# Optimization experiments

Measured on AMD Instinct MI355X. Metric: run time of the kernel, lower is better.

## Reference

```python
import jax, jax.numpy as jnp
import numpy as np

D_MODEL = 1024
NUM_HEADS = 16
HEAD_DIM = D_MODEL // NUM_HEADS


def setup_inputs() -> dict:
    key = jax.random.key(0)
    ks = jax.random.split(key, 5)
    s = 1.0 / np.sqrt(D_MODEL)
    return {
        "x": jax.random.normal(ks[0], (2, 2048, D_MODEL), dtype=jnp.float32),
        "Wqkv": jax.random.normal(ks[1], (3 * D_MODEL, D_MODEL), dtype=jnp.float32) * s,
        "bqkv": jax.random.normal(ks[2], (3 * D_MODEL,), dtype=jnp.float32) * s,
        "Wo": jax.random.normal(ks[3], (D_MODEL, D_MODEL), dtype=jnp.float32) * s,
        "bo": jax.random.normal(ks[4], (D_MODEL,), dtype=jnp.float32) * s,
    }


def reference(x, Wqkv, bqkv, Wo, bo):
    B, S, D = x.shape
    H, hd = NUM_HEADS, HEAD_DIM
    # fused QKV projection (torch Linear: x @ W.T + b)
    qkv = x @ Wqkv.T + bqkv                      # [B, S, 3D]
    qkv = qkv.reshape(B, S, H, 3 * hd).transpose(0, 2, 1, 3)  # [B, H, S, 3hd]
    q, k, v = jnp.split(qkv, 3, axis=-1)         # each [B, H, S, hd]
    scaled = jnp.einsum("bhqd,bhkd->bhqk", q, k) / jnp.sqrt(jnp.float32(hd))
    # module applies causal mask when its `mask` flag is False (the default)
    causal = jnp.tril(jnp.ones((S, S), dtype=bool))
    scaled = jnp.where(causal, scaled, -jnp.inf)
    attn = jax.nn.softmax(scaled, axis=-1)       # [B, H, S, S]
    values = jnp.einsum("bhqk,bhkd->bhqd", attn, v)  # [B, H, S, hd]
    # NOTE: original uses .reshape (not transpose-then-reshape) on the
    # [B, H, S, hd] tensor directly — reproduce that exact layout.
    values = values.reshape(B, S, H * hd)
    out = values @ Wo.T + bo                     # [B, S, D]
    return out
```

## Files before the change

### kernel.cpp

```cpp
#include <hip/hip_runtime.h>

typedef __attribute__((ext_vector_type(8))) short bf16x8;
typedef __attribute__((ext_vector_type(4))) float f32x4;

#define D_MODEL 1024
#define NHEADS 16
#define HDIM 64
#define SEQ 2048
#define BATCH 2
#define MROWS (BATCH*SEQ)
#define NQKV (3*D_MODEL)
#define QSCALE 0.1803368801111204f
#define CSTR 144

__device__ __forceinline__ unsigned short f2bf(float f) {
  unsigned int u = __float_as_uint(f);
  u += 0x7FFF + ((u >> 16) & 1);
  return (unsigned short)(u >> 16);
}
__device__ __forceinline__ unsigned int pack2bf(float a, float b) {
#if __has_builtin(__builtin_amdgcn_cvt_pk_bf16_f32)
  auto r = __builtin_amdgcn_cvt_pk_bf16_f32(a, b);
  unsigned int u; __builtin_memcpy(&u, &r, 4);
  return u;
#else
  return ((unsigned int)f2bf(b) << 16) | (unsigned int)f2bf(a);
#endif
}

__device__ __forceinline__ void gload16(const void* g, void* l) {
  __builtin_amdgcn_global_load_lds((const __attribute__((address_space(1))) void*)g,
                                   (__attribute__((address_space(3))) void*)l, 16, 0, 0);
}

#define N4_X     1048576
#define N4_WQKV   786432
#define N4_WO     262144
__global__ void cvt_all_kernel(const float4* __restrict__ x,
                               const float4* __restrict__ wqkv,
                               const float4* __restrict__ wo,
                               ushort4* __restrict__ xb,
                               ushort4* __restrict__ wqkvb,
                               ushort4* __restrict__ wob) {
  int i = blockIdx.x * blockDim.x + threadIdx.x;
  const float4* s; ushort4* d; int j;
  if (i < N4_X)                { s = x;    d = xb;    j = i; }
  else if (i < N4_X + N4_WQKV) { s = wqkv; d = wqkvb; j = i - N4_X; }
  else                         { s = wo;   d = wob;   j = i - (N4_X + N4_WQKV); }
  float4 v = s[j];
  ushort4 o;
  o.x = f2bf(v.x); o.y = f2bf(v.y); o.z = f2bf(v.z); o.w = f2bf(v.w);
  d[j] = o;
}

template<int MODE, int BM>
__global__ __launch_bounds__(256) void gemm_bt_kernel(
    const unsigned short* __restrict__ A,
    const unsigned short* __restrict__ Bm,
    const float* __restrict__ bias,
    float* __restrict__ outF,
    unsigned short* __restrict__ Qb,
    unsigned short* __restrict__ Kb,
    unsigned short* __restrict__ VTb,
    int M, int N, int K)
{
  constexpr int MI = BM / 32;
  constexpr int STG = BM*32 + 128*32;
  constexpr int SHSZ = (MODE == 0 && 128*CSTR > 2*STG) ? 128*CSTR : 2*STG;
  __shared__ __align__(16) unsigned short Sh[SHSZ];
  const int tid = threadIdx.x;
  const int wave = tid >> 6, lane = tid & 63;
  const int lm = lane & 15, quad = lane >> 4;
  const int wm = (wave >> 1) * (BM/2), wn = (wave & 1) * 64;
  const int m0 = blockIdx.y * BM, n0 = blockIdx.x * 128;

  f32x4 acc[MI][4] = {};

  auto stage_in = [&](int k0, int sb) {
    unsigned short* As = Sh + sb*STG;
    unsigned short* Bs = As + BM*32;
#pragma unroll
    for (int i = 0; i < BM/64; i++) {
      int ch = i*256 + tid;
      int r = ch >> 2, cg = (ch & 3) ^ ((r >> 1) & 3);
      gload16(&A[(size_t)(m0 + r) * K + k0 + cg*8], &As[ch*8]);
    }
#pragma unroll
    for (int i = 0; i < 2; i++) {
      int ch = i*256 + tid;
      int r = ch >> 2, cg = (ch & 3) ^ ((r >> 1) & 3);
      gload16(&Bm[(size_t)(n0 + r) * K + k0 + cg*8], &Bs[ch*8]);
    }
  };

  stage_in(0, 0);
  for (int k0 = 0; k0 < K; k0 += 32) {
    const int cur = (k0 >> 5) & 1;
    __syncthreads();
    if (k0 + 32 < K) stage_in(k0 + 32, cur ^ 1);
    const unsigned short* As = Sh + cur*STG;
    const unsigned short* Bs = As + BM*32;
    bf16x8 af[MI], bfr[4];
#pragma unroll
    for (int mi = 0; mi < MI; mi++) {
      int r = wm + mi*16 + lm;
      af[mi] = *(const bf16x8*)&As[(r*4 + (quad ^ ((r >> 1) & 3))) * 8];
    }
#pragma unroll
    for (int ni = 0; ni < 4; ni++) {
      int r = wn + ni*16 + lm;
      bfr[ni] = *(const bf16x8*)&Bs[(r*4 + (quad ^ ((r >> 1) & 3))) * 8];
    }
#pragma unroll
    for (int mi = 0; mi < MI; mi++)
#pragma unroll
      for (int ni = 0; ni < 4; ni++)
        acc[mi][ni] = __builtin_amdgcn_mfma_f32_16x16x32_bf16(af[mi], bfr[ni], acc[mi][ni], 0, 0, 0);
  }

  if (MODE == 1) {
#pragma unroll
    for (int mi = 0; mi < MI; mi++)
#pragma unroll
      for (int ni = 0; ni < 4; ni++)
#pragma unroll
        for (int r = 0; r < 4; r++) {
          int row = m0 + wm + mi*16 + quad*4 + r;
          int col = n0 + wn + ni*16 + lm;
          outF[(size_t)row * N + col] = acc[mi][ni][r] + bias[col];
        }
  } else {
    __syncthreads();
#pragma unroll
    for (int mi = 0; mi < MI; mi++)
#pragma unroll
      for (int ni = 0; ni < 4; ni++)
#pragma unroll
        for (int r = 0; r < 4; r++) {
          int row_l = wm + mi*16 + quad*4 + r;
          int col_l = wn + ni*16 + lm;
          int col = n0 + col_l;
          float v = acc[mi][ni][r] + bias[col];
          if (((col % 192) >> 6) == 0) v *= QSCALE;
          Sh[row_l*CSTR + col_l] = f2bf(v);
        }
    __syncthreads();
#pragma unroll
    for (int i = 0; i < 8; i++) {
      int lin = i*256 + tid;
      int row_l = lin >> 4, cc = (lin & 15) * 8;
      int col = n0 + cc;
      int h = col / 192, rr = col - h*192;
      int ty = rr >> 6, e = rr & 63;
      if (ty < 2) {
        uint4 d = *(const uint4*)&Sh[row_l*CSTR + cc];
        int row = m0 + row_l;
        int b = row >> 11, s = row & (SEQ - 1);
        unsigned short* dst = ty ? Kb : Qb;
        *(uint4*)&dst[((size_t)(b*NHEADS + h)*SEQ + s)*HDIM + e] = d;
      }
    }
#pragma unroll
    for (int i = 0; i < 8; i++) {
      int lin = i*256 + tid;
      int col_l = lin & 127, s8 = (lin >> 7) * 8;
      int col = n0 + col_l;
      int h = col / 192, rr = col - h*192;
      if ((rr >> 6) == 2) {
        int e = rr & 63;
        unsigned short tmp[8];
#pragma unroll
        for (int j = 0; j < 8; j++) tmp[j] = Sh[(s8 + j)*CSTR + col_l];
        int row = m0 + s8;
        int b = row >> 11, s = row & (SEQ - 1);
        size_t vb = ((size_t)(b*NHEADS + h)*HDIM + e)*SEQ;
        int pos = (s & ~31) | (((s >> 2) & 3) << 3) | (((s >> 4) & 1) << 2);
        *(uint2*)&VTb[vb + pos]     = *(const uint2*)&tmp[0];
        *(uint2*)&VTb[vb + pos + 8] = *(const uint2*)&tmp[4];
      }
    }
  }
}

__global__ __launch_bounds__(512) void flash_attn_kernel(
    const unsigned short* __restrict__ Qb,
    const unsigned short* __restrict__ Kb,
    const unsigned short* __restrict__ VTb,
    unsigned short* __restrict__ Ob)
{
  const int tid = threadIdx.x;
  const int wave = tid >> 6, lane = tid & 63;
  const int lm = lane & 15, quad = lane >> 4;
  const int bx = blockIdx.x;
  const int bh = (bx & 7) * 4 + (bx >> 3);
  const int pr = blockIdx.y;
  const int t0 = 15 - pr, t1 = pr;
  const int nk0 = t0 + 1;
  const int ntot = nk0 + t1 + 1;

  __shared__ __align__(16) unsigned short Ks[2][128*64];
  __shared__ __align__(16) unsigned short Vs[2][64*128];

  const unsigned short* Qbh  = Qb  + (size_t)bh*SEQ*HDIM;
  const unsigned short* Kbh  = Kb  + (size_t)bh*SEQ*HDIM;
  const unsigned short* VTbh = VTb + (size_t)bh*HDIM*SEQ;

  auto stage_in = [&](int k0, int sb) {
#pragma unroll
    for (int i = 0; i < 2; i++) {
      int ch = i*512 + tid;
      int r = ch >> 3, cg = (ch & 7) ^ (r & 7);
      gload16(&Kbh[(size_t)(k0 + r)*HDIM + cg*8], &Ks[sb][ch*8]);
    }
#pragma unroll
    for (int i = 0; i < 2; i++) {
      int ch = i*512 + tid;
      int e = ch >> 4, cg = (ch & 15) ^ (e & 7);
      gload16(&VTbh[(size_t)e*SEQ + k0 + cg*8], &Vs[sb][ch*8]);
    }
  };

  int rowq = t0*128 + wave*16;
  int query = rowq + lm;
  bf16x8 qf[2];
#pragma unroll
  for (int kc = 0; kc < 2; kc++)
    qf[kc] = *(const bf16x8*)&Qbh[(size_t)query*HDIM + kc*32 + quad*8];

  f32x4 o[4] = {};
  float m_run = -1e30f, l_run = 0.f;

  stage_in(0, 0);
  for (int s = 0; s < ntot; s++) {
    const int kt = (s < nk0) ? s : s - nk0;
    const int k0 = kt * 128;
    const int cur = s & 1;
    __syncthreads();
    if (s + 1 < ntot) {
      int sn = s + 1;
      int ktn = (sn < nk0) ? sn : sn - nk0;
      stage_in(ktn * 128, cur ^ 1);
    }

    f32x4 sc[8] = {};
#pragma unroll
    for (int kc = 0; kc < 2; kc++)
#pragma unroll
      for (int mi = 0; mi < 8; mi++) {
        int r = mi*16 + lm, cc = kc*4 + quad;
        bf16x8 kf = *(const bf16x8*)&Ks[cur][(r*8 + (cc ^ (r & 7))) * 8];
        sc[mi] = __builtin_amdgcn_mfma_f32_16x16x32_bf16(kf, qf[kc], sc[mi], 0, 0, 0);
      }

    if (k0 + 127 > rowq) {
#pragma unroll
      for (int mi = 0; mi < 8; mi++)
#pragma unroll
        for (int r = 0; r < 4; r++) {
          int key = k0 + mi*16 + quad*4 + r;
          if (key > query) sc[mi][r] = -1e30f;
        }
    }

    float mx = sc[0][0];
#pragma unroll
    for (int mi = 0; mi < 8; mi++)
#pragma unroll
      for (int r = 0; r < 4; r++) mx = fmaxf(mx, sc[mi][r]);
    mx = fmaxf(mx, __shfl_xor(mx, 16, 64));
    mx = fmaxf(mx, __shfl_xor(mx, 32, 64));
    float mnew = fmaxf(m_run, mx);
    float alpha = exp2f(m_run - mnew);
    float p[8][4];
    float rs = 0.f;
#pragma unroll
    for (int mi = 0; mi < 8; mi++)
#pragma unroll
      for (int r = 0; r < 4; r++) {
        p[mi][r] = exp2f(sc[mi][r] - mnew);
        rs += p[mi][r];
      }
    rs += __shfl_xor(rs, 16, 64);
    rs += __shfl_xor(rs, 32, 64);
    l_run = l_run * alpha + rs;
    if (__any(mnew != m_run)) {
#pragma unroll
      for (int ei = 0; ei < 4; ei++)
#pragma unroll
        for (int r = 0; r < 4; r++) o[ei][r] *= alpha;
    }
    m_run = mnew;

#pragma unroll
    for (int kc = 0; kc < 4; kc++) {
      union { unsigned int w[4]; bf16x8 v; } pu;
      pu.w[0] = pack2bf(p[2*kc][0],   p[2*kc][1]);
      pu.w[1] = pack2bf(p[2*kc][2],   p[2*kc][3]);
      pu.w[2] = pack2bf(p[2*kc+1][0], p[2*kc+1][1]);
      pu.w[3] = pack2bf(p[2*kc+1][2], p[2*kc+1][3]);
#pragma unroll
      for (int ei = 0; ei < 4; ei++) {
        int e = ei*16 + lm, cc = kc*4 + quad;
        bf16x8 vf = *(const bf16x8*)&Vs[cur][(e*16 + (cc ^ (e & 7))) * 8];
        o[ei] = __builtin_amdgcn_mfma_f32_16x16x32_bf16(vf, pu.v, o[ei], 0, 0, 0);
      }
    }

    if (s == nk0 - 1 || s == ntot - 1) {
      float inv = 1.0f / l_run;
      size_t obase = ((size_t)bh*SEQ + query) * HDIM;
#pragma unroll
      for (int ei = 0; ei < 4; ei++) {
        uint2 u;
        u.x = pack2bf(o[ei][0]*inv, o[ei][1]*inv);
        u.y = pack2bf(o[ei][2]*inv, o[ei][3]*inv);
        *(uint2*)&Ob[obase + ei*16 + quad*4] = u;
      }
      if (s == nk0 - 1) {
        rowq = t1*128 + wave*16;
        query = rowq + lm;
#pragma unroll
        for (int kc = 0; kc < 2; kc++)
          qf[kc] = *(const bf16x8*)&Qbh[(size_t)query*HDIM + kc*32 + quad*8];
#pragma unroll
        for (int ei = 0; ei < 4; ei++)
#pragma unroll
          for (int r = 0; r < 4; r++) o[ei][r] = 0.f;
        m_run = -1e30f; l_run = 0.f;
      }
    }
  }
}

extern "C" void kernel_launch(void* const* d_in, const int* in_sizes, int n_in,
                              void* d_out, int out_size, void* d_ws, size_t ws_size,
                              hipStream_t stream) {
  const float* x    = (const float*)d_in[0];
  const float* Wqkv = (const float*)d_in[1];
  const float* bqkv = (const float*)d_in[2];
  const float* Wo   = (const float*)d_in[3];
  const float* bo   = (const float*)d_in[4];
  float* out = (float*)d_out;

  char* ws = (char*)d_ws;
  unsigned short* Xbf    = (unsigned short*)(ws);
  unsigned short* Wqkvbf = (unsigned short*)(ws + 8388608);
  unsigned short* Wobf   = (unsigned short*)(ws + 14680064);
  unsigned short* Qb     = (unsigned short*)(ws + 16777216);
  unsigned short* Kb     = (unsigned short*)(ws + 25165824);
  unsigned short* VTb    = (unsigned short*)(ws + 33554432);
  unsigned short* Ob     = (unsigned short*)(ws + 41943040);

  cvt_all_kernel<<<8192, 256, 0, stream>>>(
      (const float4*)x, (const float4*)Wqkv, (const float4*)Wo,
      (ushort4*)Xbf, (ushort4*)Wqkvbf, (ushort4*)Wobf);

  gemm_bt_kernel<0,128><<<dim3(24, 32), 256, 0, stream>>>(
      Xbf, Wqkvbf, bqkv, nullptr, Qb, Kb, VTb, MROWS, NQKV, D_MODEL);

  flash_attn_kernel<<<dim3(32, 8), 512, 0, stream>>>(Qb, Kb, VTb, Ob);

  gemm_bt_kernel<1,64><<<dim3(8, 64), 256, 0, stream>>>(
      Ob, Wobf, bo, out, nullptr, nullptr, nullptr, MROWS, D_MODEL, D_MODEL);
}
```

Baseline: 184.3 us.

## Software-pipeline flash attention: overlap previous tile's PV with current QK

Restructures the attention loop so the P·V MFMAs for the previous key tile run after the current tile's Q·K MFMAs. The deferred rescale factor and packed probabilities are carried across iterations, and K/V staging grows from double to triple buffering so the previous tile's V stays resident. It also adds s_setprio around the MFMA blocks, rewrites the row max/sum as tree reductions, and sets launch_bounds to (512,2). The aim is to hide softmax latency behind matrix work. The cost is more registers and LDS: 96KB per block likely allows only one block per CU, which may reduce occupancy.

```diff
diff --git a/kernel.cpp b/kernel.cpp
--- a/kernel.cpp
+++ b/kernel.cpp
@@ -182,7 +182,7 @@
   }
 }
 
-__global__ __launch_bounds__(512) void flash_attn_kernel(
+__global__ __launch_bounds__(512, 2) void flash_attn_kernel(
     const unsigned short* __restrict__ Qb,
     const unsigned short* __restrict__ Kb,
     const unsigned short* __restrict__ VTb,
@@ -198,8 +198,8 @@
   const int nk0 = t0 + 1;
   const int ntot = nk0 + t1 + 1;
 
-  __shared__ __align__(16) unsigned short Ks[2][128*64];
-  __shared__ __align__(16) unsigned short Vs[2][64*128];
+  __shared__ __align__(16) unsigned short Ks[3][128*64];
+  __shared__ __align__(16) unsigned short Vs[3][64*128];
 
   const unsigned short* Qbh  = Qb  + (size_t)bh*SEQ*HDIM;
   const unsigned short* Kbh  = Kb  + (size_t)bh*SEQ*HDIM;
@@ -222,6 +222,7 @@
 
   int rowq = t0*128 + wave*16;
   int query = rowq + lm;
+  int query_ep = query;
   bf16x8 qf[2];
 #pragma unroll
   for (int kc = 0; kc < 2; kc++)
@@ -229,20 +230,26 @@
 
   f32x4 o[4] = {};
   float m_run = -1e30f, l_run = 0.f;
+  bf16x8 pf_prev[4];
+  float alpha_prev = 0.f;
+  bool resc_prev = false;
 
   stage_in(0, 0);
+  int cur = 0;
   for (int s = 0; s < ntot; s++) {
     const int kt = (s < nk0) ? s : s - nk0;
     const int k0 = kt * 128;
-    const int cur = s & 1;
+    const int prv = (cur == 0) ? 2 : cur - 1;
+    const int nxt = (cur == 2) ? 0 : cur + 1;
     __syncthreads();
     if (s + 1 < ntot) {
       int sn = s + 1;
       int ktn = (sn < nk0) ? sn : sn - nk0;
-      stage_in(ktn * 128, cur ^ 1);
+      stage_in(ktn * 128, nxt);
     }
 
     f32x4 sc[8] = {};
+    __builtin_amdgcn_s_setprio(1);
 #pragma unroll
     for (int kc = 0; kc < 2; kc++)
 #pragma unroll
@@ -251,6 +258,7 @@
         bf16x8 kf = *(const bf16x8*)&Ks[cur][(r*8 + (cc ^ (r & 7))) * 8];
         sc[mi] = __builtin_amdgcn_mfma_f32_16x16x32_bf16(kf, qf[kc], sc[mi], 0, 0, 0);
       }
+    __builtin_amdgcn_s_setprio(0);
 
     if (k0 + 127 > rowq) {
 #pragma unroll
@@ -262,35 +270,75 @@
         }
     }
 
-    float mx = sc[0][0];
+    if (s > 0) {
+      if (resc_prev) {
+#pragma unroll
+        for (int ei = 0; ei < 4; ei++)
+#pragma unroll
+          for (int r2 = 0; r2 < 4; r2++) o[ei][r2] *= alpha_prev;
+      }
+      __builtin_amdgcn_s_setprio(1);
+#pragma unroll
+      for (int kc = 0; kc < 4; kc++)
+#pragma unroll
+        for (int ei = 0; ei < 4; ei++) {
+          int e = ei*16 + lm, cc = kc*4 + quad;
+          bf16x8 vf = *(const bf16x8*)&Vs[prv][(e*16 + (cc ^ (e & 7))) * 8];
+          o[ei] = __builtin_amdgcn_mfma_f32_16x16x32_bf16(vf, pf_prev[kc], o[ei], 0, 0, 0);
+        }
+      __builtin_amdgcn_s_setprio(0);
+      if (s == nk0) {
+        float inv = 1.0f / l_run;
+        size_t obase = ((size_t)bh*SEQ + query_ep) * HDIM;
+#pragma unroll
+        for (int ei = 0; ei < 4; ei++) {
+          uint2 u;
+          u.x = pack2bf(o[ei][0]*inv, o[ei][1]*inv);
+          u.y = pack2bf(o[ei][2]*inv, o[ei][3]*inv);
+          *(uint2*)&Ob[obase + ei*16 + quad*4] = u;
+        }
+#pragma unroll
+        for (int ei = 0; ei < 4; ei++)
+#pragma unroll
+          for (int r2 = 0; r2 < 4; r2++) o[ei][r2] = 0.f;
+        m_run = -1e30f; l_run = 0.f;
+      }
+    }
+
+    float tr8[8];
 #pragma unroll
     for (int mi = 0; mi < 8; mi++)
-#pragma unroll
-      for (int r = 0; r < 4; r++) mx = fmaxf(mx, sc[mi][r]);
+      tr8[mi] = fmaxf(fmaxf(sc[mi][0], sc[mi][1]), fmaxf(sc[mi][2], sc[mi][3]));
+#pragma unroll
+    for (int st = 4; st > 0; st >>= 1)
+#pragma unroll
+      for (int j = 0; j < st; j++) tr8[j] = fmaxf(tr8[j], tr8[j + st]);
+    float mx = tr8[0];
     mx = fmaxf(mx, __shfl_xor(mx, 16, 64));
     mx = fmaxf(mx, __shfl_xor(mx, 32, 64));
     float mnew = fmaxf(m_run, mx);
     float alpha = exp2f(m_run - mnew);
     float p[8][4];
-    float rs = 0.f;
 #pragma unroll
     for (int mi = 0; mi < 8; mi++)
 #pragma unroll
-      for (int r = 0; r < 4; r++) {
-        p[mi][r] = exp2f(sc[mi][r] - mnew);
-        rs += p[mi][r];
-      }
+      for (int r2 = 0; r2 < 4; r2++)
+        p[mi][r2] = exp2f(sc[mi][r2] - mnew);
+    float sr8[8];
+#pragma unroll
+    for (int mi = 0; mi < 8; mi++)
+      sr8[mi] = (p[mi][0] + p[mi][1]) + (p[mi][2] + p[mi][3]);
+#pragma unroll
+    for (int st = 4; st > 0; st >>= 1)
+#pragma unroll
+      for (int j = 0; j < st; j++) sr8[j] += sr8[j + st];
+    float rs = sr8[0];
     rs += __shfl_xor(rs, 16, 64);
     rs += __shfl_xor(rs, 32, 64);
+    resc_prev = __any(mnew != m_run);
+    alpha_prev = alpha;
     l_run = l_run * alpha + rs;
-    if (__any(mnew != m_run)) {
-#pragma unroll
-      for (int ei = 0; ei < 4; ei++)
-#pragma unroll
-        for (int r = 0; r < 4; r++) o[ei][r] *= alpha;
-    }
     m_run = mnew;
-
 #pragma unroll
     for (int kc = 0; kc < 4; kc++) {
       union { unsigned int w[4]; bf16x8 v; } pu;
@@ -298,36 +346,44 @@
       pu.w[1] = pack2bf(p[2*kc][2],   p[2*kc][3]);
       pu.w[2] = pack2bf(p[2*kc+1][0], p[2*kc+1][1]);
       pu.w[3] = pack2bf(p[2*kc+1][2], p[2*kc+1][3]);
+      pf_prev[kc] = pu.v;
+    }
+
+    if (s == nk0 - 1) {
+      query_ep = query;
+      rowq = t1*128 + wave*16;
+      query = rowq + lm;
+#pragma unroll
+      for (int kc = 0; kc < 2; kc++)
+        qf[kc] = *(const bf16x8*)&Qbh[(size_t)query*HDIM + kc*32 + quad*8];
+    }
+    cur = nxt;
+  }
+
+  {
+    const int prv = (cur == 0) ? 2 : cur - 1;
+    if (resc_prev) {
+#pragma unroll
+      for (int ei = 0; ei < 4; ei++)
+#pragma unroll
+        for (int r2 = 0; r2 < 4; r2++) o[ei][r2] *= alpha_prev;
+    }
+#pragma unroll
+    for (int kc = 0; kc < 4; kc++)
 #pragma unroll
       for (int ei = 0; ei < 4; ei++) {
         int e = ei*16 + lm, cc = kc*4 + quad;
-        bf16x8 vf = *(const bf16x8*)&Vs[cur][(e*16 + (cc ^ (e & 7))) * 8];
-        o[ei] = __builtin_amdgcn_mfma_f32_16x16x32_bf16(vf, pu.v, o[ei], 0, 0, 0);
-      }
-    }
-
-    if (s == nk0 - 1 || s == ntot - 1) {
-      float inv = 1.0f / l_run;
-      size_t obase = ((size_t)bh*SEQ + query) * HDIM;
-#pragma unroll
-      for (int ei = 0; ei < 4; ei++) {
-        uint2 u;
-        u.x = pack2bf(o[ei][0]*inv, o[ei][1]*inv);
-        u.y = pack2bf(o[ei][2]*inv, o[ei][3]*inv);
-        *(uint2*)&Ob[obase + ei*16 + quad*4] = u;
-      }
-      if (s == nk0 - 1) {
-        rowq = t1*128 + wave*16;
-        query = rowq + lm;
-#pragma unroll
-        for (int kc = 0; kc < 2; kc++)
-          qf[kc] = *(const bf16x8*)&Qbh[(size_t)query*HDIM + kc*32 + quad*8];
-#pragma unroll
-        for (int ei = 0; ei < 4; ei++)
-#pragma unroll
-          for (int r = 0; r < 4; r++) o[ei][r] = 0.f;
-        m_run = -1e30f; l_run = 0.f;
-      }
+        bf16x8 vf = *(const bf16x8*)&Vs[prv][(e*16 + (cc ^ (e & 7))) * 8];
+        o[ei] = __builtin_amdgcn_mfma_f32_16x16x32_bf16(vf, pf_prev[kc], o[ei], 0, 0, 0);
+      }
+    float inv = 1.0f / l_run;
+    size_t obase = ((size_t)bh*SEQ + query) * HDIM;
+#pragma unroll
+    for (int ei = 0; ei < 4; ei++) {
+      uint2 u;
+      u.x = pack2bf(o[ei][0]*inv, o[ei][1]*inv);
+      u.y = pack2bf(o[ei][2]*inv, o[ei][3]*inv);
+      *(uint2*)&Ob[obase + ei*16 + quad*4] = u;
     }
   }
 }
```

After: 189.0 us. +2.5%, slower.

## Split paired causal tiles into separate blocks and add MFMA priority hints

Applied to the files above, without the earlier changes.

The attention grid no longer has each block process a pair of query tiles (a long one and a short one). It now launches one block per query tile, with heavy tiles scheduled first, which doubles the grid from 256 to 512 blocks. It also adds s_setprio around the MFMA loops, tree-structured max and sum reductions, and launch_bounds(512,4) to limit register use. The aim is more parallelism and occupancy and a shorter critical path in the softmax. The cost is less even work per block and possible register spills under the tighter launch bound.

```diff
diff --git a/kernel.cpp b/kernel.cpp
--- a/kernel.cpp
+++ b/kernel.cpp
@@ -182,7 +182,7 @@
   }
 }
 
-__global__ __launch_bounds__(512) void flash_attn_kernel(
+__global__ __launch_bounds__(512, 4) void flash_attn_kernel(
     const unsigned short* __restrict__ Qb,
     const unsigned short* __restrict__ Kb,
     const unsigned short* __restrict__ VTb,
@@ -193,10 +193,9 @@
   const int lm = lane & 15, quad = lane >> 4;
   const int bx = blockIdx.x;
   const int bh = (bx & 7) * 4 + (bx >> 3);
-  const int pr = blockIdx.y;
-  const int t0 = 15 - pr, t1 = pr;
-  const int nk0 = t0 + 1;
-  const int ntot = nk0 + t1 + 1;
+  const int by = blockIdx.y;
+  const int t  = (by < 8) ? (15 - by) : (by - 8);
+  const int nk = t + 1;
 
   __shared__ __align__(16) unsigned short Ks[2][128*64];
   __shared__ __align__(16) unsigned short Vs[2][64*128];
@@ -220,8 +219,8 @@
     }
   };
 
-  int rowq = t0*128 + wave*16;
-  int query = rowq + lm;
+  const int rowq = t*128 + wave*16;
+  const int query = rowq + lm;
   bf16x8 qf[2];
 #pragma unroll
   for (int kc = 0; kc < 2; kc++)
@@ -231,18 +230,14 @@
   float m_run = -1e30f, l_run = 0.f;
 
   stage_in(0, 0);
-  for (int s = 0; s < ntot; s++) {
-    const int kt = (s < nk0) ? s : s - nk0;
-    const int k0 = kt * 128;
+  for (int s = 0; s < nk; s++) {
+    const int k0 = s * 128;
     const int cur = s & 1;
     __syncthreads();
-    if (s + 1 < ntot) {
-      int sn = s + 1;
-      int ktn = (sn < nk0) ? sn : sn - nk0;
-      stage_in(ktn * 128, cur ^ 1);
-    }
+    if (s + 1 < nk) stage_in(k0 + 128, cur ^ 1);
 
     f32x4 sc[8] = {};
+    __builtin_amdgcn_s_setprio(1);
 #pragma unroll
     for (int kc = 0; kc < 2; kc++)
 #pragma unroll
@@ -251,6 +246,7 @@
         bf16x8 kf = *(const bf16x8*)&Ks[cur][(r*8 + (cc ^ (r & 7))) * 8];
         sc[mi] = __builtin_amdgcn_mfma_f32_16x16x32_bf16(kf, qf[kc], sc[mi], 0, 0, 0);
       }
+    __builtin_amdgcn_s_setprio(0);
 
     if (k0 + 127 > rowq) {
 #pragma unroll
@@ -262,24 +258,34 @@
         }
     }
 
-    float mx = sc[0][0];
+    float tr8[8];
 #pragma unroll
     for (int mi = 0; mi < 8; mi++)
-#pragma unroll
-      for (int r = 0; r < 4; r++) mx = fmaxf(mx, sc[mi][r]);
+      tr8[mi] = fmaxf(fmaxf(sc[mi][0], sc[mi][1]), fmaxf(sc[mi][2], sc[mi][3]));
+#pragma unroll
+    for (int st = 4; st > 0; st >>= 1)
+#pragma unroll
+      for (int j = 0; j < st; j++) tr8[j] = fmaxf(tr8[j], tr8[j + st]);
+    float mx = tr8[0];
     mx = fmaxf(mx, __shfl_xor(mx, 16, 64));
     mx = fmaxf(mx, __shfl_xor(mx, 32, 64));
     float mnew = fmaxf(m_run, mx);
     float alpha = exp2f(m_run - mnew);
     float p[8][4];
-    float rs = 0.f;
 #pragma unroll
     for (int mi = 0; mi < 8; mi++)
 #pragma unroll
-      for (int r = 0; r < 4; r++) {
-        p[mi][r] = exp2f(sc[mi][r] - mnew);
-        rs += p[mi][r];
-      }
+      for (int r2 = 0; r2 < 4; r2++)
+        p[mi][r2] = exp2f(sc[mi][r2] - mnew);
+    float sr8[8];
+#pragma unroll
+    for (int mi = 0; mi < 8; mi++)
+      sr8[mi] = (p[mi][0] + p[mi][1]) + (p[mi][2] + p[mi][3]);
+#pragma unroll
+    for (int st = 4; st > 0; st >>= 1)
+#pragma unroll
+      for (int j = 0; j < st; j++) sr8[j] += sr8[j + st];
+    float rs = sr8[0];
     rs += __shfl_xor(rs, 16, 64);
     rs += __shfl_xor(rs, 32, 64);
     l_run = l_run * alpha + rs;
@@ -287,10 +293,11 @@
 #pragma unroll
       for (int ei = 0; ei < 4; ei++)
 #pragma unroll
-        for (int r = 0; r < 4; r++) o[ei][r] *= alpha;
+        for (int r2 = 0; r2 < 4; r2++) o[ei][r2] *= alpha;
     }
     m_run = mnew;
 
+    __builtin_amdgcn_s_setprio(1);
 #pragma unroll
     for (int kc = 0; kc < 4; kc++) {
       union { unsigned int w[4]; bf16x8 v; } pu;
@@ -305,29 +312,18 @@
         o[ei] = __builtin_amdgcn_mfma_f32_16x16x32_bf16(vf, pu.v, o[ei], 0, 0, 0);
       }
     }
-
-    if (s == nk0 - 1 || s == ntot - 1) {
-      float inv = 1.0f / l_run;
-      size_t obase = ((size_t)bh*SEQ + query) * HDIM;
-#pragma unroll
-      for (int ei = 0; ei < 4; ei++) {
-        uint2 u;
-        u.x = pack2bf(o[ei][0]*inv, o[ei][1]*inv);
-        u.y = pack2bf(o[ei][2]*inv, o[ei][3]*inv);
-        *(uint2*)&Ob[obase + ei*16 + quad*4] = u;
-      }
-      if (s == nk0 - 1) {
-        rowq = t1*128 + wave*16;
-        query = rowq + lm;
-#pragma unroll
-        for (int kc = 0; kc < 2; kc++)
-          qf[kc] = *(const bf16x8*)&Qbh[(size_t)query*HDIM + kc*32 + quad*8];
-#pragma unroll
-        for (int ei = 0; ei < 4; ei++)
-#pragma unroll
-          for (int r = 0; r < 4; r++) o[ei][r] = 0.f;
-        m_run = -1e30f; l_run = 0.f;
-      }
+    __builtin_amdgcn_s_setprio(0);
+  }
+
+  {
+    float inv = 1.0f / l_run;
+    size_t obase = ((size_t)bh*SEQ + query) * HDIM;
+#pragma unroll
+    for (int ei = 0; ei < 4; ei++) {
+      uint2 u;
+      u.x = pack2bf(o[ei][0]*inv, o[ei][1]*inv);
+      u.y = pack2bf(o[ei][2]*inv, o[ei][3]*inv);
+      *(uint2*)&Ob[obase + ei*16 + quad*4] = u;
     }
   }
 }
@@ -358,7 +354,7 @@
   gemm_bt_kernel<0,128><<<dim3(24, 32), 256, 0, stream>>>(
       Xbf, Wqkvbf, bqkv, nullptr, Qb, Kb, VTb, MROWS, NQKV, D_MODEL);
 
-  flash_attn_kernel<<<dim3(32, 8), 512, 0, stream>>>(Qb, Kb, VTb, Ob);
+  flash_attn_kernel<<<dim3(32, 16), 512, 0, stream>>>(Qb, Kb, VTb, Ob);
 
   gemm_bt_kernel<1,64><<<dim3(8, 64), 256, 0, stream>>>(
       Ob, Wobf, bo, out, nullptr, nullptr, nullptr, MROWS, D_MODEL, D_MODEL);
```

Measured after the change: 184.0 us. No clear change (-0.2%).

## Split each attention key tile across wave pairs and merge partial softmax states

Applied to the files above, without the earlier changes.

The flash attention block grows from 8 to 16 waves. Each pair of waves shares a 16-query slice, and each wave of the pair handles half of the 128-key tile. The two partial (m, l, O) states are merged through shared-memory scratch at the end of each query tile, and s_setprio raises priority around the MFMA sections. This is meant to add waves in flight to hide latency and halve per-wave register pressure. In exchange it adds a scratch buffer, an extra block barrier with merge arithmetic, and redundant per-wave softmax bookkeeping.

```diff
diff --git a/kernel.cpp b/kernel.cpp
--- a/kernel.cpp
+++ b/kernel.cpp
@@ -182,7 +182,7 @@
   }
 }
 
-__global__ __launch_bounds__(512) void flash_attn_kernel(
+__global__ __launch_bounds__(1024, 4) void flash_attn_kernel(
     const unsigned short* __restrict__ Qb,
     const unsigned short* __restrict__ Kb,
     const unsigned short* __restrict__ VTb,
@@ -191,6 +191,8 @@
   const int tid = threadIdx.x;
   const int wave = tid >> 6, lane = tid & 63;
   const int lm = lane & 15, quad = lane >> 4;
+  const int qg = wave >> 1;
+  const int kh = wave & 1;
   const int bx = blockIdx.x;
   const int bh = (bx & 7) * 4 + (bx >> 3);
   const int pr = blockIdx.y;
@@ -198,29 +200,27 @@
   const int nk0 = t0 + 1;
   const int ntot = nk0 + t1 + 1;
 
-  __shared__ __align__(16) unsigned short Ks[2][128*64];
-  __shared__ __align__(16) unsigned short Vs[2][64*128];
+  __shared__ __align__(16) unsigned short Sh[2][128*64 + 64*128];
+  __shared__ __align__(16) float Scr[8*64*18];
 
   const unsigned short* Qbh  = Qb  + (size_t)bh*SEQ*HDIM;
   const unsigned short* Kbh  = Kb  + (size_t)bh*SEQ*HDIM;
   const unsigned short* VTbh = VTb + (size_t)bh*HDIM*SEQ;
 
   auto stage_in = [&](int k0, int sb) {
-#pragma unroll
-    for (int i = 0; i < 2; i++) {
-      int ch = i*512 + tid;
+    {
+      int ch = tid;
       int r = ch >> 3, cg = (ch & 7) ^ (r & 7);
-      gload16(&Kbh[(size_t)(k0 + r)*HDIM + cg*8], &Ks[sb][ch*8]);
-    }
-#pragma unroll
-    for (int i = 0; i < 2; i++) {
-      int ch = i*512 + tid;
+      gload16(&Kbh[(size_t)(k0 + r)*HDIM + cg*8], &Sh[sb][ch*8]);
+    }
+    {
+      int ch = tid;
       int e = ch >> 4, cg = (ch & 15) ^ (e & 7);
-      gload16(&VTbh[(size_t)e*SEQ + k0 + cg*8], &Vs[sb][ch*8]);
+      gload16(&VTbh[(size_t)e*SEQ + k0 + cg*8], &Sh[sb][128*64 + ch*8]);
     }
   };
 
-  int rowq = t0*128 + wave*16;
+  int rowq = t0*128 + qg*16;
   int query = rowq + lm;
   bf16x8 qf[2];
 #pragma unroll
@@ -241,45 +241,52 @@
       int ktn = (sn < nk0) ? sn : sn - nk0;
       stage_in(ktn * 128, cur ^ 1);
     }
-
-    f32x4 sc[8] = {};
+    const unsigned short* Ksc = &Sh[cur][0];
+    const unsigned short* Vsc = &Sh[cur][128*64];
+
+    f32x4 sc[4] = {};
+    __builtin_amdgcn_s_setprio(1);
 #pragma unroll
     for (int kc = 0; kc < 2; kc++)
 #pragma unroll
-      for (int mi = 0; mi < 8; mi++) {
-        int r = mi*16 + lm, cc = kc*4 + quad;
-        bf16x8 kf = *(const bf16x8*)&Ks[cur][(r*8 + (cc ^ (r & 7))) * 8];
+      for (int mi = 0; mi < 4; mi++) {
+        int r = (kh*4 + mi)*16 + lm, cc = kc*4 + quad;
+        bf16x8 kf = *(const bf16x8*)&Ksc[(r*8 + (cc ^ (r & 7))) * 8];
         sc[mi] = __builtin_amdgcn_mfma_f32_16x16x32_bf16(kf, qf[kc], sc[mi], 0, 0, 0);
       }
-
-    if (k0 + 127 > rowq) {
-#pragma unroll
-      for (int mi = 0; mi < 8; mi++)
+    __builtin_amdgcn_s_setprio(0);
+
+    if (k0 + kh*64 + 63 > rowq) {
+#pragma unroll
+      for (int mi = 0; mi < 4; mi++)
 #pragma unroll
         for (int r = 0; r < 4; r++) {
-          int key = k0 + mi*16 + quad*4 + r;
+          int key = k0 + (kh*4 + mi)*16 + quad*4 + r;
           if (key > query) sc[mi][r] = -1e30f;
         }
     }
 
-    float mx = sc[0][0];
-#pragma unroll
-    for (int mi = 0; mi < 8; mi++)
-#pragma unroll
-      for (int r = 0; r < 4; r++) mx = fmaxf(mx, sc[mi][r]);
+    float tr4[4];
+#pragma unroll
+    for (int mi = 0; mi < 4; mi++)
+      tr4[mi] = fmaxf(fmaxf(fmaxf(sc[mi][0], sc[mi][1]), sc[mi][2]), sc[mi][3]);
+    float mx = fmaxf(fmaxf(tr4[0], tr4[1]), fmaxf(tr4[2], tr4[3]));
     mx = fmaxf(mx, __shfl_xor(mx, 16, 64));
     mx = fmaxf(mx, __shfl_xor(mx, 32, 64));
     float mnew = fmaxf(m_run, mx);
+    float mq = fmaxf(mnew, -1e20f);
     float alpha = exp2f(m_run - mnew);
-    float p[8][4];
-    float rs = 0.f;
-#pragma unroll
-    for (int mi = 0; mi < 8; mi++)
-#pragma unroll
-      for (int r = 0; r < 4; r++) {
-        p[mi][r] = exp2f(sc[mi][r] - mnew);
-        rs += p[mi][r];
-      }
+    float p[4][4];
+#pragma unroll
+    for (int mi = 0; mi < 4; mi++)
+#pragma unroll
+      for (int r2 = 0; r2 < 4; r2++)
+        p[mi][r2] = exp2f(sc[mi][r2] - mq);
+    float sr4[4];
+#pragma unroll
+    for (int mi = 0; mi < 4; mi++)
+      sr4[mi] = (p[mi][0] + p[mi][1]) + (p[mi][2] + p[mi][3]);
+    float rs = (sr4[0] + sr4[1]) + (sr4[2] + sr4[3]);
     rs += __shfl_xor(rs, 16, 64);
     rs += __shfl_xor(rs, 32, 64);
     l_run = l_run * alpha + rs;
@@ -287,37 +294,58 @@
 #pragma unroll
       for (int ei = 0; ei < 4; ei++)
 #pragma unroll
-        for (int r = 0; r < 4; r++) o[ei][r] *= alpha;
+        for (int r2 = 0; r2 < 4; r2++) o[ei][r2] *= alpha;
     }
     m_run = mnew;
 
-#pragma unroll
-    for (int kc = 0; kc < 4; kc++) {
+    __builtin_amdgcn_s_setprio(1);
+#pragma unroll
+    for (int c = 0; c < 2; c++) {
       union { unsigned int w[4]; bf16x8 v; } pu;
-      pu.w[0] = pack2bf(p[2*kc][0],   p[2*kc][1]);
-      pu.w[1] = pack2bf(p[2*kc][2],   p[2*kc][3]);
-      pu.w[2] = pack2bf(p[2*kc+1][0], p[2*kc+1][1]);
-      pu.w[3] = pack2bf(p[2*kc+1][2], p[2*kc+1][3]);
+      pu.w[0] = pack2bf(p[2*c][0],   p[2*c][1]);
+      pu.w[1] = pack2bf(p[2*c][2],   p[2*c][3]);
+      pu.w[2] = pack2bf(p[2*c+1][0], p[2*c+1][1]);
+      pu.w[3] = pack2bf(p[2*c+1][2], p[2*c+1][3]);
 #pragma unroll
       for (int ei = 0; ei < 4; ei++) {
-        int e = ei*16 + lm, cc = kc*4 + quad;
-        bf16x8 vf = *(const bf16x8*)&Vs[cur][(e*16 + (cc ^ (e & 7))) * 8];
+        int e = ei*16 + lm, cc = (2*kh + c)*4 + quad;
+        bf16x8 vf = *(const bf16x8*)&Vsc[(e*16 + (cc ^ (e & 7))) * 8];
         o[ei] = __builtin_amdgcn_mfma_f32_16x16x32_bf16(vf, pu.v, o[ei], 0, 0, 0);
       }
     }
+    __builtin_amdgcn_s_setprio(0);
 
     if (s == nk0 - 1 || s == ntot - 1) {
-      float inv = 1.0f / l_run;
-      size_t obase = ((size_t)bh*SEQ + query) * HDIM;
-#pragma unroll
-      for (int ei = 0; ei < 4; ei++) {
-        uint2 u;
-        u.x = pack2bf(o[ei][0]*inv, o[ei][1]*inv);
-        u.y = pack2bf(o[ei][2]*inv, o[ei][3]*inv);
-        *(uint2*)&Ob[obase + ei*16 + quad*4] = u;
+      float* mine = Scr + (qg*64 + lane)*18;
+      if (kh) {
+        mine[0] = m_run; mine[1] = l_run;
+#pragma unroll
+        for (int ei = 0; ei < 4; ei++)
+#pragma unroll
+          for (int r2 = 0; r2 < 4; r2++) mine[2 + ei*4 + r2] = o[ei][r2];
+      }
+      __syncthreads();
+      if (!kh) {
+        float mB = mine[0], lB = mine[1];
+        float mS = fmaxf(m_run, mB);
+        float aA = exp2f(m_run - mS), aB = exp2f(mB - mS);
+        float inv = 1.0f / (l_run * aA + lB * aB);
+        float sA = aA * inv, sB = aB * inv;
+        size_t obase = ((size_t)bh*SEQ + query) * HDIM;
+#pragma unroll
+        for (int ei = 0; ei < 4; ei++) {
+          float v0 = o[ei][0]*sA + mine[2 + ei*4 + 0]*sB;
+          float v1 = o[ei][1]*sA + mine[2 + ei*4 + 1]*sB;
+          float v2 = o[ei][2]*sA + mine[2 + ei*4 + 2]*sB;
+          float v3 = o[ei][3]*sA + mine[2 + ei*4 + 3]*sB;
+          uint2 u;
+          u.x = pack2bf(v0, v1);
+          u.y = pack2bf(v2, v3);
+          *(uint2*)&Ob[obase + ei*16 + quad*4] = u;
+        }
       }
       if (s == nk0 - 1) {
-        rowq = t1*128 + wave*16;
+        rowq = t1*128 + qg*16;
         query = rowq + lm;
 #pragma unroll
         for (int kc = 0; kc < 2; kc++)
@@ -325,7 +353,7 @@
 #pragma unroll
         for (int ei = 0; ei < 4; ei++)
 #pragma unroll
-          for (int r = 0; r < 4; r++) o[ei][r] = 0.f;
+          for (int r2 = 0; r2 < 4; r2++) o[ei][r2] = 0.f;
         m_run = -1e30f; l_run = 0.f;
       }
     }
@@ -358,7 +386,7 @@
   gemm_bt_kernel<0,128><<<dim3(24, 32), 256, 0, stream>>>(
       Xbf, Wqkvbf, bqkv, nullptr, Qb, Kb, VTb, MROWS, NQKV, D_MODEL);
 
-  flash_attn_kernel<<<dim3(32, 8), 512, 0, stream>>>(Qb, Kb, VTb, Ob);
+  flash_attn_kernel<<<dim3(32, 8), 1024, 0, stream>>>(Qb, Kb, VTb, Ob);
 
   gemm_bt_kernel<1,64><<<dim3(8, 64), 256, 0, stream>>>(
       Ob, Wobf, bo, out, nullptr, nullptr, nullptr, MROWS, D_MODEL, D_MODEL);
```

Result: no change. 185.6 us (+0.7%).
